# Performance work log

Measured on AMD Instinct MI355X. Metric: run time of the kernel, lower is better.

Reference implementation:

```python
import jax, jax.numpy as jnp
import numpy as np

B, T, P, I, H, O = 64, 32, 64, 256, 128, 88  # batch, time_steps, pitch_steps, input, hidden, output


def setup_inputs() -> dict:
    key = jax.random.key(0)
    ks = jax.random.split(key, 11)
    s = 0.05
    return {
        "x": jax.random.normal(ks[0], (B, T, P, I), jnp.float32),
        # stacked [fwd, bwd] direction weights, PyTorch LSTM gate order (i, f, g, o)
        "Wt_ih": jax.random.normal(ks[1], (2, 4 * H, I), jnp.float32) * s,
        "Wt_hh": jax.random.normal(ks[2], (2, 4 * H, H), jnp.float32) * s,
        "bt_ih": jax.random.normal(ks[3], (2, 4 * H), jnp.float32) * s,
        "bt_hh": jax.random.normal(ks[4], (2, 4 * H), jnp.float32) * s,
        "Wp_ih": jax.random.normal(ks[5], (2, 4 * H, 2 * H), jnp.float32) * s,
        "Wp_hh": jax.random.normal(ks[6], (2, 4 * H, H), jnp.float32) * s,
        "bp_ih": jax.random.normal(ks[7], (2, 4 * H), jnp.float32) * s,
        "bp_hh": jax.random.normal(ks[8], (2, 4 * H), jnp.float32) * s,
        "Wo": jax.random.normal(ks[9], (O, 2 * H), jnp.float32) * s,
        "bo": jax.random.normal(ks[10], (O,), jnp.float32) * s,
    }


def _cell(xt, h, c, Wih, Whh, bih, bhh):
    # PyTorch LSTMCell math, gate order i, f, g, o
    g = xt @ Wih.T + h @ Whh.T + bih + bhh  # [B, 4H]
    i, f, gc, o = jnp.split(g, 4, axis=-1)
    c2 = jax.nn.sigmoid(f) * c + jax.nn.sigmoid(i) * jnp.tanh(gc)
    h2 = jax.nn.sigmoid(o) * jnp.tanh(c2)
    return h2, c2


def reference(x, Wt_ih, Wt_hh, bt_ih, bt_hh, Wp_ih, Wp_hh, bp_ih, bp_hh, Wo, bo):
    b = x.shape[0]
    xs = x.reshape(b, T * P, I).transpose(1, 0, 2)  # [T*P, B, I] grid flattened in (t, p) order
    z = jnp.zeros((b, H), x.dtype)
    carry0 = (z, z, z, z, z, z, z, z)

    def step(carry, xt):
        htf, ctf, htb, ctb, hpf, cpf, hpb, cpb = carry
        # time LSTM: seq_len==1 so both directions see the same single step, state carried across grid
        htf, ctf = _cell(xt, htf, ctf, Wt_ih[0], Wt_hh[0], bt_ih[0], bt_hh[0])
        htb, ctb = _cell(xt, htb, ctb, Wt_ih[1], Wt_hh[1], bt_ih[1], bt_hh[1])
        tout = jnp.concatenate([htf, htb], axis=-1)  # [B, 2H]
        # pitch LSTM consumes time_out
        hpf, cpf = _cell(tout, hpf, cpf, Wp_ih[0], Wp_hh[0], bp_ih[0], bp_hh[0])
        hpb, cpb = _cell(tout, hpb, cpb, Wp_ih[1], Wp_hh[1], bp_ih[1], bp_hh[1])
        return (htf, ctf, htb, ctb, hpf, cpf, hpb, cpb), None

    carry, _ = jax.lax.scan(step, carry0, xs)
    pitch_out = jnp.concatenate([carry[4], carry[6]], axis=-1)  # last-step pitch output [B, 2H]
    return pitch_out @ Wo.T + bo  # [B, O]
```

## Files before the change

kernel.cpp:

```cpp
#include <hip/hip_runtime.h>
#include <hip/hip_fp16.h>
#include <stdint.h>


typedef _Float16 f16;
typedef _Float16 f16x4 __attribute__((ext_vector_type(4)));
typedef _Float16 f16x8 __attribute__((ext_vector_type(8)));
typedef float f32x4 __attribute__((ext_vector_type(4)));

#if defined(__has_builtin)
#if __has_builtin(__builtin_amdgcn_rcpf)
#define FRCP(x) __builtin_amdgcn_rcpf(x)
#else
#define FRCP(x) (1.f / (x))
#endif
#if __has_builtin(__builtin_amdgcn_exp2f)
#define FEXP2(x) __builtin_amdgcn_exp2f(x)
#else
#define FEXP2(x) __exp2f(x)
#endif
#endif

#define K_SIG 1.4426950409f
#define K_TANH 2.8853900818f


__global__ __launch_bounds__(256) void k_convert_x(const float* __restrict__ x,
                                                   f16* __restrict__ xh) {
    size_t id = (size_t)blockIdx.x * 256 + threadIdx.x;
    const float4* src = (const float4*)(x + id * 8);
    float4 v0 = src[0], v1 = src[1];
    f16x8 o = {(f16)v0.x, (f16)v0.y, (f16)v0.z, (f16)v0.w,
               (f16)v1.x, (f16)v1.y, (f16)v1.z, (f16)v1.w};
    *(f16x8*)(xh + id * 8) = o;
}

__global__ __launch_bounds__(256) void k_convert_wp(const float* __restrict__ src,
                                                    f16* __restrict__ dst, int ksh, int n8) {
    int id = blockIdx.x * 256 + threadIdx.x;
    if (id >= n8) return;
    int rp = id >> ksh;
    int kb = id & ((1 << ksh) - 1);
    int dd = rp >> 9, gi = rp & 3, q = (rp >> 2) & 127;
    float sc = (gi == 2) ? K_TANH : K_SIG;
    size_t so = ((size_t)(dd * 512 + gi * 128 + q) << (ksh + 3)) + kb * 8;
    const float4* sp = (const float4*)(src + so);
    float4 v0 = sp[0], v1 = sp[1];
    f16x8 o = {(f16)(v0.x * sc), (f16)(v0.y * sc), (f16)(v0.z * sc), (f16)(v0.w * sc),
               (f16)(v1.x * sc), (f16)(v1.y * sc), (f16)(v1.z * sc), (f16)(v1.w * sc)};
    *(f16x8*)(dst + (size_t)id * 8) = o;
}

__global__ __launch_bounds__(256) void k_bias(const float* __restrict__ a,
                                              const float* __restrict__ b,
                                              float* __restrict__ o) {
    int rp = blockIdx.x * 256 + threadIdx.x;
    int dd = rp >> 9, gi = rp & 3, q = (rp >> 2) & 127;
    int orig = dd * 512 + gi * 128 + q;
    float sc = (gi == 2) ? K_TANH : K_SIG;
    o[rp] = (a[orig] + b[orig]) * sc;
}


#define BM 128
#define BN 128
#define BKK 32
#define LDT 40

__global__ __launch_bounds__(256) void k_gemm(const f16* __restrict__ A,
                                              const f16* __restrict__ B,
                                              f16* __restrict__ C,
                                              const float* __restrict__ bsum,
                                              int M, int N, int K) {
    __shared__ __align__(16) f16 As[BM * LDT];
    __shared__ __align__(16) f16 Bs[BN * LDT];
    const int tid  = threadIdx.x;
    const int m0   = blockIdx.x * BM;
    const int n0   = blockIdx.y * BN;
    const int lane = tid & 63;
    const int wave = tid >> 6;
    const int wm   = (wave & 1) * 64;
    const int wn   = (wave >> 1) * 64;
    const int r    = tid >> 1;
    const int koff = (tid & 1) * 16;
    const int mrow = lane & 15;
    const int kof  = (lane >> 4) * 8;
    const int crow = (lane >> 4) * 4;

    f32x4 acc[4][4];
#pragma unroll
    for (int i = 0; i < 4; ++i)
#pragma unroll
        for (int j = 0; j < 4; ++j) acc[i][j] = (f32x4){0.f, 0.f, 0.f, 0.f};

    for (int k0 = 0; k0 < K; k0 += BKK) {
        uint4 a0 = *(const uint4*)(A + (size_t)(m0 + r) * K + k0 + koff);
        uint4 a1 = *(const uint4*)(A + (size_t)(m0 + r) * K + k0 + koff + 8);
        uint4 b0 = *(const uint4*)(B + (size_t)(n0 + r) * K + k0 + koff);
        uint4 b1 = *(const uint4*)(B + (size_t)(n0 + r) * K + k0 + koff + 8);
        *(uint4*)(As + r * LDT + koff)     = a0;
        *(uint4*)(As + r * LDT + koff + 8) = a1;
        *(uint4*)(Bs + r * LDT + koff)     = b0;
        *(uint4*)(Bs + r * LDT + koff + 8) = b1;
        __syncthreads();
        f16x8 af[4], bfr[4];
#pragma unroll
        for (int i = 0; i < 4; ++i)
            af[i] = *(const f16x8*)(As + (wm + i * 16 + mrow) * LDT + kof);
#pragma unroll
        for (int j = 0; j < 4; ++j)
            bfr[j] = *(const f16x8*)(Bs + (wn + j * 16 + mrow) * LDT + kof);
#pragma unroll
        for (int i = 0; i < 4; ++i)
#pragma unroll
            for (int j = 0; j < 4; ++j)
                acc[i][j] = __builtin_amdgcn_mfma_f32_16x16x32_f16(af[i], bfr[j], acc[i][j], 0, 0, 0);
        __syncthreads();
    }
#pragma unroll
    for (int i = 0; i < 4; ++i) {
        const int rb = m0 + wm + i * 16 + crow;
        const float4 bbv = *(const float4*)(bsum + rb);
        const int dd = rb >> 9;
        const int uu = (rb & 511) >> 2;
#pragma unroll
        for (int j = 0; j < 4; ++j) {
            const int cm = n0 + wn + j * 16 + (lane & 15);
            const int b  = cm >> 11;
            const int s  = cm & 2047;
            f16x4 v = {(f16)(acc[i][j][0] + bbv.x), (f16)(acc[i][j][1] + bbv.y),
                       (f16)(acc[i][j][2] + bbv.z), (f16)(acc[i][j][3] + bbv.w)};
            size_t fofs = ((((size_t)b * 256 + (s >> 3)) * 2 + dd) * 128 + uu) * 32
                          + (s & 7) * 4;
            *(f16x4*)(C + fofs) = v;
        }
    }
}


template <int MODE>
__global__ void __attribute__((amdgpu_flat_work_group_size(512, 512),
                               amdgpu_waves_per_eu(2, 2))) k_lstm(
    const f16* __restrict__ G,
    const f16* __restrict__ Whh,
    f16* __restrict__ tout,
    float* __restrict__ hfin,
    const int S) {
    const int wg = blockIdx.x;
    const int b  = wg >> 1, d = wg & 1;
    const int t  = threadIdx.x;
    const int l  = t & 63, wv = t >> 6;
    const int hi = l >> 4, ch = l & 15;
    const int tau = ch & 3;

    __shared__ __align__(16) f16 ring[16][128];

    f16x8 w[4][4];
#pragma unroll
    for (int tt = 0; tt < 4; ++tt)
#pragma unroll
        for (int ks = 0; ks < 4; ++ks)
            w[tt][ks] = *(const f16x8*)(Whh + ((size_t)d * 512 + (4 * wv + tt) * 16 + ch) * 128
                                        + ks * 32 + hi * 8);

    for (int i = t; i < 1024; i += 512) ((uint32_t*)ring)[i] = 0;

    const int u = 16 * wv + 4 * tau + hi;
    const f16* gp = G + ((((size_t)b * 256) * 2 + d) * 128 + u) * 32;

    uint4 gc[4], gn[4];
#pragma unroll
    for (int q = 0; q < 4; ++q) gc[q] = *(const uint4*)(gp + q * 8);

    const f32x4 Z = {0.f, 0.f, 0.f, 0.f};
    float c = 0.f;
    __syncthreads();

    for (int sb = 0; sb < S; sb += 8) {
        {
            const size_t nb = (size_t)((sb + 8 < S) ? (sb >> 3) + 1 : (sb >> 3));
#pragma unroll
            for (int q = 0; q < 4; ++q) gn[q] = *(const uint4*)(gp + nb * 8192 + q * 8);
        }
        if (MODE == 1 && sb > 0 && t < 256) {
            const int jf = t >> 5, of = t & 31;
            uint2 hv = *(const uint2*)(&ring[((sb - 8) & 15) + jf][of * 4]);
            *(uint2*)(tout + ((size_t)b * 2048 + (sb - 8 + jf)) * 256 + d * 128 + of * 4) = hv;
        }
#pragma unroll
        for (int j8 = 0; j8 < 8; ++j8) {
            const int s = sb + j8;
            const f16* hb = &ring[(s + 15) & 15][0];
            f16x8 b0 = *(const f16x8*)(hb + hi * 8);
            f16x8 b1 = *(const f16x8*)(hb + 32 + hi * 8);
            f16x8 b2 = *(const f16x8*)(hb + 64 + hi * 8);
            f16x8 b3 = *(const f16x8*)(hb + 96 + hi * 8);
            f32x4 A0 = __builtin_amdgcn_mfma_f32_16x16x32_f16(w[0][0], b0, Z, 0, 0, 0);
            f32x4 A1 = __builtin_amdgcn_mfma_f32_16x16x32_f16(w[1][0], b0, Z, 0, 0, 0);
            f32x4 A2 = __builtin_amdgcn_mfma_f32_16x16x32_f16(w[2][0], b0, Z, 0, 0, 0);
            f32x4 A3 = __builtin_amdgcn_mfma_f32_16x16x32_f16(w[3][0], b0, Z, 0, 0, 0);
            A0 = __builtin_amdgcn_mfma_f32_16x16x32_f16(w[0][1], b1, A0, 0, 0, 0);
            A1 = __builtin_amdgcn_mfma_f32_16x16x32_f16(w[1][1], b1, A1, 0, 0, 0);
            A2 = __builtin_amdgcn_mfma_f32_16x16x32_f16(w[2][1], b1, A2, 0, 0, 0);
            A3 = __builtin_amdgcn_mfma_f32_16x16x32_f16(w[3][1], b1, A3, 0, 0, 0);
            A0 = __builtin_amdgcn_mfma_f32_16x16x32_f16(w[0][2], b2, A0, 0, 0, 0);
            A1 = __builtin_amdgcn_mfma_f32_16x16x32_f16(w[1][2], b2, A1, 0, 0, 0);
            A2 = __builtin_amdgcn_mfma_f32_16x16x32_f16(w[2][2], b2, A2, 0, 0, 0);
            A3 = __builtin_amdgcn_mfma_f32_16x16x32_f16(w[3][2], b2, A3, 0, 0, 0);
            A0 = __builtin_amdgcn_mfma_f32_16x16x32_f16(w[0][3], b3, A0, 0, 0, 0);
            A1 = __builtin_amdgcn_mfma_f32_16x16x32_f16(w[1][3], b3, A1, 0, 0, 0);
            A2 = __builtin_amdgcn_mfma_f32_16x16x32_f16(w[2][3], b3, A2, 0, 0, 0);
            A3 = __builtin_amdgcn_mfma_f32_16x16x32_f16(w[3][3], b3, A3, 0, 0, 0);
            uint2 gpair;
            if ((j8 & 1) == 0) { gpair.x = gc[j8 >> 1].x; gpair.y = gc[j8 >> 1].y; }
            else               { gpair.x = gc[j8 >> 1].z; gpair.y = gc[j8 >> 1].w; }
            f16x4 gf = __builtin_bit_cast(f16x4, gpair);
            const bool s0 = (ch & 1) != 0;
            const bool s1 = (ch & 2) != 0;
            float v0, v1, v2, v3;
            {
                float x, y;
                x = s0 ? A1[0] : A0[0]; y = s0 ? A3[0] : A2[0]; v0 = (s1 ? y : x) + (float)gf[0];
                x = s0 ? A1[1] : A0[1]; y = s0 ? A3[1] : A2[1]; v1 = (s1 ? y : x) + (float)gf[1];
                x = s0 ? A1[2] : A0[2]; y = s0 ? A3[2] : A2[2]; v2 = (s1 ? y : x) + (float)gf[2];
                x = s0 ? A1[3] : A0[3]; y = s0 ? A3[3] : A2[3]; v3 = (s1 ? y : x) + (float)gf[3];
            }
            float si = FRCP(1.f + FEXP2(-v0));
            float sf = FRCP(1.f + FEXP2(-v1));
            float tg = __builtin_fmaf(-2.f, FRCP(1.f + FEXP2(v2)), 1.f);
            float so = FRCP(1.f + FEXP2(-v3));
            c = __builtin_fmaf(sf, c, si * tg);
            float tc = __builtin_fmaf(-2.f, FRCP(1.f + FEXP2(c * K_TANH)), 1.f);
            float hv = so * tc;
            if (ch < 4) ring[s & 15][u] = (f16)hv;
            if (MODE == 2 && s == S - 1 && ch < 4)
                hfin[(size_t)b * 256 + d * 128 + u] = hv;
            __asm__ __volatile__("s_waitcnt lgkmcnt(0)\n\ts_barrier" ::: "memory");
        }
#pragma unroll
        for (int q = 0; q < 4; ++q) gc[q] = gn[q];
    }
    if (MODE == 1 && t < 256) {
        const int jf = t >> 5, of = t & 31;
        uint2 hv = *(const uint2*)(&ring[((S - 8) & 15) + jf][of * 4]);
        *(uint2*)(tout + ((size_t)b * 2048 + (S - 8 + jf)) * 256 + d * 128 + of * 4) = hv;
    }
}


__global__ __launch_bounds__(128) void k_out(const float* __restrict__ hp,
                                             const float* __restrict__ Wo,
                                             const float* __restrict__ bo,
                                             float* __restrict__ out) {
    const int b = blockIdx.x;
    const int t = threadIdx.x;
    __shared__ float hs[256];
    hs[t] = hp[b * 256 + t];
    hs[t + 128] = hp[b * 256 + 128 + t];
    __syncthreads();
    if (t < 88) {
        float acc = bo[t];
        const float* wr = Wo + t * 256;
#pragma unroll 4
        for (int k = 0; k < 256; ++k) acc += wr[k] * hs[k];
        out[b * 88 + t] = acc;
    }
}


extern "C" void kernel_launch(void* const* d_in, const int* in_sizes, int n_in,
                              void* d_out, int out_size, void* d_ws, size_t ws_size,
                              hipStream_t stream) {
    const float* x    = (const float*)d_in[0];
    const float* Wtih = (const float*)d_in[1];
    const float* Wthh = (const float*)d_in[2];
    const float* btih = (const float*)d_in[3];
    const float* bthh = (const float*)d_in[4];
    const float* Wpih = (const float*)d_in[5];
    const float* Wphh = (const float*)d_in[6];
    const float* bpih = (const float*)d_in[7];
    const float* bphh = (const float*)d_in[8];
    const float* Wo   = (const float*)d_in[9];
    const float* bo   = (const float*)d_in[10];

    char* ws = (char*)d_ws;
    f16*   xh    = (f16*)(ws + 0);
    f16*   G     = (f16*)(ws + 67108864);
    f16*   tout  = (f16*)(ws + 335544320);
    f16*   wtih  = (f16*)(ws + 402653184);
    f16*   wthh  = (f16*)(ws + 403177472);
    f16*   wpih  = (f16*)(ws + 403439616);
    f16*   wphh  = (f16*)(ws + 403963904);
    float* bsT   = (float*)(ws + 404226048);
    float* bsP   = (float*)(ws + 404230144);
    float* hp    = (float*)(ws + 404226048);

    k_convert_x<<<16384, 256, 0, stream>>>(x, xh);
    k_convert_wp<<<128, 256, 0, stream>>>(Wtih, wtih, 5, 32768);
    k_convert_wp<<<64,  256, 0, stream>>>(Wthh, wthh, 4, 16384);
    k_convert_wp<<<128, 256, 0, stream>>>(Wpih, wpih, 5, 32768);
    k_convert_wp<<<64,  256, 0, stream>>>(Wphh, wphh, 4, 16384);
    k_bias<<<4, 256, 0, stream>>>(btih, bthh, bsT);
    k_bias<<<4, 256, 0, stream>>>(bpih, bphh, bsP);

    k_gemm<<<dim3(8, 1024), 256, 0, stream>>>(wtih, xh, G, bsT, 1024, 131072, 256);
    k_lstm<1><<<128, 512, 0, stream>>>(G, wthh, tout, nullptr, 2048);
    k_gemm<<<dim3(8, 1024), 256, 0, stream>>>(wpih, tout, G, bsP, 1024, 131072, 256);
    k_lstm<2><<<128, 512, 0, stream>>>(G, wphh, nullptr, hp, 2048);
    k_out<<<64, 128, 0, stream>>>(hp, Wo, bo, (float*)d_out);
}
```

Measured before the change: 2.388 ms.

## Spread LSTM gate activations across lanes with DPP quad broadcast

Reassigns the recurrent LSTM lanes so each of four lanes in a quad evaluates one gate's nonlinearity, then uses DPP quad_perm broadcasts to gather i, f, g and o for the cell update. Sigmoid gate weights and biases are pre-scaled by -log2(e), so a single exp2/rcp plus one FMA gives either sigmoid or tanh per lane, replacing four transcendental evaluations per lane. Ring buffer addressing is also hoisted to per-block base pointers. The cost is extra select and DPP instructions on the serial per-step critical path.

```diff
diff --git a/kernel.cpp b/kernel.cpp
--- a/kernel.cpp
+++ b/kernel.cpp
@@ -24,6 +24,12 @@
 #define K_SIG 1.4426950409f
 #define K_TANH 2.8853900818f
 
+template <int CTRL>
+static __device__ __forceinline__ float qperm(float v) {
+    int r = __builtin_amdgcn_update_dpp(0, __builtin_bit_cast(int, v), CTRL, 0xf, 0xf, true);
+    return __builtin_bit_cast(float, r);
+}
+
 
 __global__ __launch_bounds__(256) void k_convert_x(const float* __restrict__ x,
                                                    f16* __restrict__ xh) {
@@ -42,7 +48,7 @@
     int rp = id >> ksh;
     int kb = id & ((1 << ksh) - 1);
     int dd = rp >> 9, gi = rp & 3, q = (rp >> 2) & 127;
-    float sc = (gi == 2) ? K_TANH : K_SIG;
+    float sc = (gi == 2) ? K_TANH : -K_SIG;
     size_t so = ((size_t)(dd * 512 + gi * 128 + q) << (ksh + 3)) + kb * 8;
     const float4* sp = (const float4*)(src + so);
     float4 v0 = sp[0], v1 = sp[1];
@@ -57,7 +63,7 @@
     int rp = blockIdx.x * 256 + threadIdx.x;
     int dd = rp >> 9, gi = rp & 3, q = (rp >> 2) & 127;
     int orig = dd * 512 + gi * 128 + q;
-    float sc = (gi == 2) ? K_TANH : K_SIG;
+    float sc = (gi == 2) ? K_TANH : -K_SIG;
     o[rp] = (a[orig] + b[orig]) * sc;
 }
 
@@ -151,22 +157,30 @@
     const int t  = threadIdx.x;
     const int l  = t & 63, wv = t >> 6;
     const int hi = l >> 4, ch = l & 15;
-    const int tau = ch & 3;
+    const int tt = ch >> 2, g = ch & 3;
 
     __shared__ __align__(16) f16 ring[16][128];
 
     f16x8 w[4][4];
 #pragma unroll
-    for (int tt = 0; tt < 4; ++tt)
+    for (int q = 0; q < 4; ++q)
 #pragma unroll
         for (int ks = 0; ks < 4; ++ks)
-            w[tt][ks] = *(const f16x8*)(Whh + ((size_t)d * 512 + (4 * wv + tt) * 16 + ch) * 128
-                                        + ks * 32 + hi * 8);
+            w[q][ks] = *(const f16x8*)(Whh + ((size_t)d * 512 + (4 * wv + q) * 16 + ch) * 128
+                                       + ks * 32 + hi * 8);
 
     for (int i = t; i < 1024; i += 512) ((uint32_t*)ring)[i] = 0;
 
-    const int u = 16 * wv + 4 * tau + hi;
+    const int u = (4 * wv + tt) * 4 + hi;
     const f16* gp = G + ((((size_t)b * 256) * 2 + d) * 128 + u) * 32;
+
+    const bool t0 = (tt & 1) != 0, t1 = (tt & 2) != 0;
+    const bool r0 = (g & 1) != 0, r1 = (g & 2) != 0;
+    const bool pG = (g & 2) != 0;
+    const int  shG = (g & 1) * 16;
+    const float Aact = (g == 2) ? 1.f : 0.f;
+    const float Bact = (g == 2) ? -2.f : 1.f;
+    const bool wrt = (g == 0);
 
     uint4 gc[4], gn[4];
 #pragma unroll
@@ -187,14 +201,18 @@
             uint2 hv = *(const uint2*)(&ring[((sb - 8) & 15) + jf][of * 4]);
             *(uint2*)(tout + ((size_t)b * 2048 + (sb - 8 + jf)) * 256 + d * 128 + of * 4) = hv;
         }
-#pragma unroll
-        for (int j8 = 0; j8 < 8; ++j8) {
-            const int s = sb + j8;
-            const f16* hb = &ring[(s + 15) & 15][0];
-            f16x8 b0 = *(const f16x8*)(hb + hi * 8);
-            f16x8 b1 = *(const f16x8*)(hb + 32 + hi * 8);
-            f16x8 b2 = *(const f16x8*)(hb + 64 + hi * 8);
-            f16x8 b3 = *(const f16x8*)(hb + 96 + hi * 8);
+        const int half = sb & 15;
+        const f16* rd0 = &ring[(half ^ 8) + 7][hi * 8];
+        const f16* rdc = &ring[half][hi * 8];
+        f16* wrp = &ring[half][u];
+#pragma unroll
+        for (int jj = 0; jj < 8; ++jj) {
+            const int s = sb + jj;
+            const f16* hb = (jj == 0) ? rd0 : (rdc + (jj - 1) * 128);
+            f16x8 b0 = *(const f16x8*)(hb);
+            f16x8 b1 = *(const f16x8*)(hb + 32);
+            f16x8 b2 = *(const f16x8*)(hb + 64);
+            f16x8 b3 = *(const f16x8*)(hb + 96);
             f32x4 A0 = __builtin_amdgcn_mfma_f32_16x16x32_f16(w[0][0], b0, Z, 0, 0, 0);
             f32x4 A1 = __builtin_amdgcn_mfma_f32_16x16x32_f16(w[1][0], b0, Z, 0, 0, 0);
             f32x4 A2 = __builtin_amdgcn_mfma_f32_16x16x32_f16(w[2][0], b0, Z, 0, 0, 0);
@@ -211,29 +229,31 @@
             A1 = __builtin_amdgcn_mfma_f32_16x16x32_f16(w[1][3], b3, A1, 0, 0, 0);
             A2 = __builtin_amdgcn_mfma_f32_16x16x32_f16(w[2][3], b3, A2, 0, 0, 0);
             A3 = __builtin_amdgcn_mfma_f32_16x16x32_f16(w[3][3], b3, A3, 0, 0, 0);
-            uint2 gpair;
-            if ((j8 & 1) == 0) { gpair.x = gc[j8 >> 1].x; gpair.y = gc[j8 >> 1].y; }
-            else               { gpair.x = gc[j8 >> 1].z; gpair.y = gc[j8 >> 1].w; }
-            f16x4 gf = __builtin_bit_cast(f16x4, gpair);
-            const bool s0 = (ch & 1) != 0;
-            const bool s1 = (ch & 2) != 0;
-            float v0, v1, v2, v3;
-            {
-                float x, y;
-                x = s0 ? A1[0] : A0[0]; y = s0 ? A3[0] : A2[0]; v0 = (s1 ? y : x) + (float)gf[0];
-                x = s0 ? A1[1] : A0[1]; y = s0 ? A3[1] : A2[1]; v1 = (s1 ? y : x) + (float)gf[1];
-                x = s0 ? A1[2] : A0[2]; y = s0 ? A3[2] : A2[2]; v2 = (s1 ? y : x) + (float)gf[2];
-                x = s0 ? A1[3] : A0[3]; y = s0 ? A3[3] : A2[3]; v3 = (s1 ? y : x) + (float)gf[3];
+            f32x4 X, Y, T;
+#pragma unroll
+            for (int e = 0; e < 4; ++e) {
+                X[e] = t0 ? A1[e] : A0[e];
+                Y[e] = t0 ? A3[e] : A2[e];
+                T[e] = t1 ? Y[e] : X[e];
             }
-            float si = FRCP(1.f + FEXP2(-v0));
-            float sf = FRCP(1.f + FEXP2(-v1));
-            float tg = __builtin_fmaf(-2.f, FRCP(1.f + FEXP2(v2)), 1.f);
-            float so = FRCP(1.f + FEXP2(-v3));
-            c = __builtin_fmaf(sf, c, si * tg);
+            float xx = r0 ? T[1] : T[0];
+            float yy = r0 ? T[3] : T[2];
+            float v  = r1 ? yy : xx;
+            uint32_t dw0 = (jj & 1) ? gc[jj >> 1].z : gc[jj >> 1].x;
+            uint32_t dw1 = (jj & 1) ? gc[jj >> 1].w : gc[jj >> 1].y;
+            uint32_t dsel = pG ? dw1 : dw0;
+            v += (float)__builtin_bit_cast(f16, (uint16_t)(dsel >> shG));
+            float wv_ = FRCP(1.f + FEXP2(v));
+            float act = __builtin_fmaf(Bact, wv_, Aact);
+            float gi = qperm<0x00>(act);
+            float gf = qperm<0x55>(act);
+            float gg = qperm<0xAA>(act);
+            float go = qperm<0xFF>(act);
+            c = __builtin_fmaf(gf, c, gi * gg);
             float tc = __builtin_fmaf(-2.f, FRCP(1.f + FEXP2(c * K_TANH)), 1.f);
-            float hv = so * tc;
-            if (ch < 4) ring[s & 15][u] = (f16)hv;
-            if (MODE == 2 && s == S - 1 && ch < 4)
+            float hv = go * tc;
+            if (wrt) *(wrp + jj * 128) = (f16)hv;
+            if (MODE == 2 && s == S - 1 && wrt)
                 hfin[(size_t)b * 256 + d * 128 + u] = hv;
             __asm__ __volatile__("s_waitcnt lgkmcnt(0)\n\ts_barrier" ::: "memory");
         }
```

Result: no change. 2.359 ms (-1.2%).
